# Kernel tuning notes

Measured on AMD Instinct MI355X. Metric: run time of the kernel, lower is better.

Reference implementation:

```python
import jax, jax.numpy as jnp
import numpy as np

N_NODES = 100000
N_EDGES = 1600000
IN_DIM, HID_DIM, OUT_DIM = 128, 64, 64
NEG_SLOPE = 0.2


def _gat_layer(h_in, src, dst, W, a_src, a_dst, b, n_nodes):
    # h: [N, F_out]
    h = h_in @ W.T
    alpha_src = h @ a_src  # [N]
    alpha_dst = h @ a_dst  # [N]
    # per-edge raw attention logits (edge j->i: src=j, dst=i)
    e = jax.nn.leaky_relu(alpha_src[src] + alpha_dst[dst], NEG_SLOPE)  # [E]
    # segment softmax over incoming edges of each dst node
    m = jax.ops.segment_max(e, dst, num_segments=n_nodes)
    ex = jnp.exp(e - m[dst])
    denom = jax.ops.segment_sum(ex, dst, num_segments=n_nodes)
    alpha = ex / denom[dst]  # [E], denom > 0 thanks to self-loops
    out = jax.ops.segment_sum(h[src] * alpha[:, None], dst, num_segments=n_nodes)
    return out + b


def setup_inputs() -> dict:
    key = jax.random.key(0)
    ks = jax.random.split(key, 12)
    x = jax.random.normal(ks[0], (N_NODES, IN_DIM), dtype=jnp.float32)
    edge_index = jax.random.randint(ks[1], (2, N_EDGES), 0, N_NODES)
    edge_attr = jax.random.normal(ks[2], (N_EDGES, 1), dtype=jnp.float32)
    s1 = 1.0 / np.sqrt(IN_DIM)
    s2 = 1.0 / np.sqrt(HID_DIM)
    W1 = jax.random.normal(ks[3], (HID_DIM, IN_DIM), dtype=jnp.float32) * s1
    att_src1 = jax.random.normal(ks[4], (HID_DIM,), dtype=jnp.float32) * s2
    att_dst1 = jax.random.normal(ks[5], (HID_DIM,), dtype=jnp.float32) * s2
    b1 = jnp.zeros((HID_DIM,), dtype=jnp.float32)
    W2 = jax.random.normal(ks[6], (OUT_DIM, HID_DIM), dtype=jnp.float32) * s2
    att_src2 = jax.random.normal(ks[7], (OUT_DIM,), dtype=jnp.float32) * s2
    att_dst2 = jax.random.normal(ks[8], (OUT_DIM,), dtype=jnp.float32) * s2
    b2 = jnp.zeros((OUT_DIM,), dtype=jnp.float32)
    return {"x": x, "edge_index": edge_index, "edge_attr": edge_attr,
            "W1": W1, "att_src1": att_src1, "att_dst1": att_dst1, "b1": b1,
            "W2": W2, "att_src2": att_src2, "att_dst2": att_dst2, "b2": b2}


def reference(x, edge_index, edge_attr, W1, att_src1, att_dst1, b1,
              W2, att_src2, att_dst2, b2):
    n = x.shape[0]
    # add self-loops (PyG GATConv default); edge_attr unused (edge_dim=None)
    loop = jnp.arange(n, dtype=edge_index.dtype)
    src = jnp.concatenate([edge_index[0], loop])
    dst = jnp.concatenate([edge_index[1], loop])
    h = _gat_layer(x, src, dst, W1, att_src1, att_dst1, b1, n)
    h = jax.nn.relu(h)
    h = _gat_layer(h, src, dst, W2, att_src2, att_dst2, b2, n)
    # global_mean_pool with batch=None -> mean over all nodes, shape [1, F]
    return jnp.mean(h, axis=0, keepdims=True)
```

## Files before the change

kernel.cpp:

```cpp
#include <hip/hip_runtime.h>

#define NEG_SLOPE 0.2f
#define BSHIFT 6
#define NBMAX 2048
#define BCAP 1408
#define CHUNK 8192

__device__ __forceinline__ unsigned short f2b(float x) {
    unsigned u = __float_as_uint(x);
    u += 0x7fff + ((u >> 16) & 1);
    return (unsigned short)(u >> 16);
}
__device__ __forceinline__ float b2f(unsigned short u) {
    return __uint_as_float((unsigned)u << 16);
}

__global__ __launch_bounds__(256) void bin_fixed_kernel(
    const int* __restrict__ ei, int* __restrict__ bcnt,
    int* __restrict__ binned, int E, int NB)
{
    __shared__ int cnt1[NBMAX], rsv[NBMAX], cnt2[NBMAX];
    const int tid = threadIdx.x;
    for (int i = tid; i < NB; i += 256) { cnt1[i] = 0; cnt2[i] = 0; }
    __syncthreads();
    const int start = blockIdx.x * CHUNK;
    const int end = min(start + CHUNK, E);
    for (int i = start + tid; i < end; i += 256)
        atomicAdd(&cnt1[ei[E + i] >> BSHIFT], 1);
    __syncthreads();
    for (int i = tid; i < NB; i += 256)
        rsv[i] = cnt1[i] ? atomicAdd(&bcnt[i], cnt1[i]) : 0;
    __syncthreads();
    for (int i = start + tid; i < end; i += 256) {
        int s = ei[i], d = ei[E + i];
        int b = d >> BSHIFT;
        int r = rsv[b] + atomicAdd(&cnt2[b], 1);
        if (r < BCAP) binned[(size_t)b * BCAP + r] = (s << BSHIFT) | (d & 63);
    }
}

__global__ __launch_bounds__(256) void bscan_kernel(
    const int* __restrict__ bcnt, int* __restrict__ bbase, int NB)
{
    __shared__ int lds[256];
    const int t = threadIdx.x;
    int v[8]; int s = 0;
    #pragma unroll
    for (int j = 0; j < 8; ++j) {
        int i = t * 8 + j;
        v[j] = (i < NB) ? bcnt[i] : 0;
        s += v[j];
    }
    lds[t] = s;
    __syncthreads();
    #pragma unroll
    for (int off = 1; off < 256; off <<= 1) {
        int x = (t >= off) ? lds[t - off] : 0;
        __syncthreads();
        lds[t] += x;
        __syncthreads();
    }
    int excl = (t > 0) ? lds[t - 1] : 0;
    #pragma unroll
    for (int j = 0; j < 8; ++j) {
        int i = t * 8 + j;
        if (i < NB) { bbase[i] = excl + 64 * i; excl += v[j]; }
    }
}

__global__ __launch_bounds__(256) void bucket_csr_kernel(
    const int* __restrict__ binned, const int* __restrict__ bcnt,
    const int* __restrict__ bbase, int* __restrict__ row_ptr,
    int* __restrict__ esrc, int N)
{
    __shared__ int ldeg[64];
    __shared__ int lcur[64];
    const int b = blockIdx.x;
    const int tid = threadIdx.x;
    const int node0 = b << BSHIFT;
    const int cnt = min(bcnt[b], BCAP);
    const int base_e = bbase[b];
    const int* bp = binned + (size_t)b * BCAP;

    if (tid < 64) ldeg[tid] = (node0 + tid < N) ? 1 : 0;
    __syncthreads();
    for (int i = tid; i < cnt; i += 256)
        atomicAdd(&ldeg[bp[i] & 63], 1);
    __syncthreads();
    if (tid < 64) {
        int v = ldeg[tid];
        int inc = v;
        #pragma unroll
        for (int off = 1; off < 64; off <<= 1) {
            int t2 = __shfl_up(inc, off, 64);
            if (tid >= off) inc += t2;
        }
        int excl = inc - v;
        int node = node0 + tid;
        if (node <= N) row_ptr[node] = base_e + excl;
        if (node < N) {
            esrc[base_e + excl] = node;
            lcur[tid] = base_e + excl + 1;
        }
    }
    __syncthreads();
    for (int i = tid; i < cnt; i += 256) {
        int v = bp[i];
        int pos = atomicAdd(&lcur[v & 63], 1);
        esrc[pos] = v >> BSHIFT;
    }
}

template<int K>
__global__ __launch_bounds__(256) void gemm_attn_kernel(
    const float* __restrict__ in, const float* __restrict__ W,
    const float* __restrict__ a_src, const float* __restrict__ a_dst,
    unsigned short* __restrict__ hb, float* __restrict__ asrc,
    float* __restrict__ adst, int N)
{
    constexpr int KB = 64;
    constexpr int NKC = KB / 4;
    constexpr int LDN = 65;
    __shared__ float4 xs4[NKC * LDN];
    __shared__ float4 ws4[NKC * LDN];
    __shared__ float avs[64], avd[64];

    const int tid = threadIdx.x;
    const int node0 = blockIdx.x * 64;
    const int tf = tid & 15;
    const int tn = tid >> 4;

    if (tid < 64) { avs[tid] = a_src[tid]; avd[tid] = a_dst[tid]; }

    float acc[4][4] = {};

    for (int k0 = 0; k0 < K; k0 += KB) {
        if (k0) __syncthreads();
        for (int i = tid; i < 64 * NKC; i += 256) {
            int r = i >> 4, kc = i & 15;
            int node = node0 + r;
            float4 xv = (node < N)
                ? *(const float4*)&in[(size_t)node * K + k0 + 4 * kc]
                : make_float4(0.f, 0.f, 0.f, 0.f);
            xs4[kc * LDN + r] = xv;
            ws4[kc * LDN + r] = *(const float4*)&W[(size_t)r * K + k0 + 4 * kc];
        }
        __syncthreads();

        #pragma unroll 4
        for (int kc = 0; kc < NKC; ++kc) {
            float4 xv[4], wv[4];
            #pragma unroll
            for (int i = 0; i < 4; ++i) xv[i] = xs4[kc * LDN + 4 * tn + i];
            #pragma unroll
            for (int j = 0; j < 4; ++j) wv[j] = ws4[kc * LDN + tf + 16 * j];
            #pragma unroll
            for (int i = 0; i < 4; ++i)
                #pragma unroll
                for (int j = 0; j < 4; ++j) {
                    acc[i][j] = fmaf(xv[i].x, wv[j].x, acc[i][j]);
                    acc[i][j] = fmaf(xv[i].y, wv[j].y, acc[i][j]);
                    acc[i][j] = fmaf(xv[i].z, wv[j].z, acc[i][j]);
                    acc[i][j] = fmaf(xv[i].w, wv[j].w, acc[i][j]);
                }
        }
    }

    #pragma unroll
    for (int i = 0; i < 4; ++i) {
        const int node = node0 + 4 * tn + i;
        const bool valid = node < N;
        float vs = 0.f, vd = 0.f;
        #pragma unroll
        for (int j = 0; j < 4; ++j) {
            int f = tf + 16 * j;
            if (valid) hb[(size_t)node * 64 + f] = f2b(acc[i][j]);
            vs = fmaf(acc[i][j], avs[f], vs);
            vd = fmaf(acc[i][j], avd[f], vd);
        }
        #pragma unroll
        for (int off = 8; off >= 1; off >>= 1) {
            vs += __shfl_down(vs, off, 16);
            vd += __shfl_down(vd, off, 16);
        }
        if (tf == 0 && valid) { asrc[node] = vs; adst[node] = vd; }
    }
}

__global__ __launch_bounds__(256) void aggregate_csr_kernel(
    const int* __restrict__ row_ptr, const int* __restrict__ esrc,
    const float* __restrict__ asrc, const float* __restrict__ adst,
    const unsigned short* __restrict__ hb, const float* __restrict__ bias,
    float* __restrict__ g, int N, int do_relu)
{
    const int node = (int)((blockIdx.x * 256 + threadIdx.x) >> 4);
    const int lane = threadIdx.x & 15;
    if (node >= N) return;
    const int beg = row_ptr[node];
    const int end = row_ptr[node + 1];
    const float ad = adst[node];
    float a0 = 0.f, a1 = 0.f, a2 = 0.f, a3 = 0.f, wsum = 0.f;
    int p = beg;
    for (; p + 4 <= end; p += 4) {
        int s[4]; ushort4 r[4]; float l[4];
        #pragma unroll
        for (int j = 0; j < 4; ++j) s[j] = esrc[p + j];
        #pragma unroll
        for (int j = 0; j < 4; ++j)
            r[j] = *(const ushort4*)(hb + (size_t)s[j] * 64 + lane * 4);
        #pragma unroll
        for (int j = 0; j < 4; ++j) l[j] = asrc[s[j]] + ad;
        #pragma unroll
        for (int j = 0; j < 4; ++j) {
            float ll = (l[j] > 0.f) ? l[j] : NEG_SLOPE * l[j];
            float w = __expf(ll);
            wsum += w;
            a0 = fmaf(w, b2f(r[j].x), a0);
            a1 = fmaf(w, b2f(r[j].y), a1);
            a2 = fmaf(w, b2f(r[j].z), a2);
            a3 = fmaf(w, b2f(r[j].w), a3);
        }
    }
    for (; p < end; ++p) {
        int s = esrc[p];
        ushort4 r = *(const ushort4*)(hb + (size_t)s * 64 + lane * 4);
        float l = asrc[s] + ad;
        l = (l > 0.f) ? l : NEG_SLOPE * l;
        float w = __expf(l);
        wsum += w;
        a0 = fmaf(w, b2f(r.x), a0);
        a1 = fmaf(w, b2f(r.y), a1);
        a2 = fmaf(w, b2f(r.z), a2);
        a3 = fmaf(w, b2f(r.w), a3);
    }
    const float inv = 1.0f / wsum;
    float4 v = make_float4(a0 * inv, a1 * inv, a2 * inv, a3 * inv);
    if (bias) {
        v.x += bias[lane * 4 + 0]; v.y += bias[lane * 4 + 1];
        v.z += bias[lane * 4 + 2]; v.w += bias[lane * 4 + 3];
    }
    if (do_relu) {
        v.x = fmaxf(v.x, 0.f); v.y = fmaxf(v.y, 0.f);
        v.z = fmaxf(v.z, 0.f); v.w = fmaxf(v.w, 0.f);
    }
    *(float4*)&g[(size_t)node * 64 + lane * 4] = v;
}

__global__ __launch_bounds__(256) void pool_kernel(
    const float* __restrict__ g, const float* __restrict__ b2,
    float* __restrict__ out, int N)
{
    __shared__ float red[256];
    const int f = threadIdx.x & 63;
    const int sub = threadIdx.x >> 6;
    float acc = 0.f;
    for (int n = blockIdx.x * 4 + sub; n < N; n += gridDim.x * 4)
        acc += g[(size_t)n * 64 + f];
    red[threadIdx.x] = acc;
    __syncthreads();
    if (threadIdx.x < 64) {
        float s = red[f] + red[64 + f] + red[128 + f] + red[192 + f];
        atomicAdd(out + f, s * (1.0f / (float)N));
        if (blockIdx.x == 0) atomicAdd(out + f, b2[f]);
    }
}

extern "C" void kernel_launch(void* const* d_in, const int* in_sizes, int n_in,
                              void* d_out, int out_size, void* d_ws, size_t ws_size,
                              hipStream_t stream) {
    const float* x   = (const float*)d_in[0];
    const int*   ei  = (const int*)d_in[1];
    const float* W1  = (const float*)d_in[3];
    const float* as1 = (const float*)d_in[4];
    const float* ad1 = (const float*)d_in[5];
    const float* b1  = (const float*)d_in[6];
    const float* W2  = (const float*)d_in[7];
    const float* as2 = (const float*)d_in[8];
    const float* ad2 = (const float*)d_in[9];
    const float* b2  = (const float*)d_in[10];
    float* out = (float*)d_out;

    const int N = in_sizes[0] / 128;
    const int E = in_sizes[1] / 2;
    const int Etot = E + N;
    const int NB = (N + 63) >> BSHIFT;

    auto align4 = [](size_t v) { return (v + 3) & ~(size_t)3; };
    float* ws    = (float*)d_ws;
    size_t off = 0;
    unsigned short* hb = (unsigned short*)(ws + off); off += align4((size_t)N * 32);
    float* g     = ws + off; off += align4((size_t)N * 64);
    float* asrc  = ws + off; off += align4(N);
    float* adst  = ws + off; off += align4(N);
    int* row_ptr = (int*)(ws + off); off += align4(N + 1);
    int* bcnt    = (int*)(ws + off); off += NBMAX;
    int* bbase   = (int*)(ws + off); off += NBMAX;
    int* esrc    = (int*)(ws + off); off += align4(Etot);
    int* binned  = (int*)g;

    const int gemm_blocks  = (N + 63) / 64;
    const int chunk_blocks = (E + CHUNK - 1) / CHUNK;
    const int agg_blocks   = (int)(((size_t)N * 16 + 255) / 256);

    hipMemsetAsync(out, 0, 64 * sizeof(float), stream);
    hipMemsetAsync(bcnt, 0, NB * sizeof(int), stream);

    bin_fixed_kernel<<<chunk_blocks, 256, 0, stream>>>(ei, bcnt, binned, E, NB);
    bscan_kernel<<<1, 256, 0, stream>>>(bcnt, bbase, NB);
    bucket_csr_kernel<<<NB, 256, 0, stream>>>(binned, bcnt, bbase, row_ptr, esrc, N);

    gemm_attn_kernel<128><<<gemm_blocks, 256, 0, stream>>>(x, W1, as1, ad1, hb, asrc, adst, N);
    aggregate_csr_kernel<<<agg_blocks, 256, 0, stream>>>(row_ptr, esrc, asrc, adst, hb, b1, g, N, 1);

    gemm_attn_kernel<64><<<gemm_blocks, 256, 0, stream>>>(g, W2, as2, ad2, hb, asrc, adst, N);
    aggregate_csr_kernel<<<agg_blocks, 256, 0, stream>>>(row_ptr, esrc, asrc, adst, hb, nullptr, g, N, 0);

    pool_kernel<<<512, 256, 0, stream>>>(g, b2, out, N);
}
```

Baseline: 311.9 us.

## Bin edges with global atomics and register-prefetch next GEMM K-chunk

The LDS-histogram chunked binning kernel becomes a one-thread-per-edge kernel that takes bucket slots directly from global atomics, and the bucket scan now clamps each count to the bucket capacity. Separately, the GEMM kernel loads the next K-chunk of inputs and weights into registers while it computes the current chunk, so global-load latency overlaps with the FMAs. The binning change trades per-block LDS reservation for heavy global atomic contention on about 1563 bucket counters, and edge order inside a bucket becomes nondeterministic. The prefetch raises register use, which may lower occupancy.

```diff
diff --git a/kernel.cpp b/kernel.cpp
--- a/kernel.cpp
+++ b/kernel.cpp
@@ -4,7 +4,6 @@
 #define BSHIFT 6
 #define NBMAX 2048
 #define BCAP 1408
-#define CHUNK 8192
 
 __device__ __forceinline__ unsigned short f2b(float x) {
     unsigned u = __float_as_uint(x);
@@ -15,28 +14,16 @@
     return __uint_as_float((unsigned)u << 16);
 }
 
-__global__ __launch_bounds__(256) void bin_fixed_kernel(
+__global__ __launch_bounds__(256) void bin_global_kernel(
     const int* __restrict__ ei, int* __restrict__ bcnt,
-    int* __restrict__ binned, int E, int NB)
-{
-    __shared__ int cnt1[NBMAX], rsv[NBMAX], cnt2[NBMAX];
-    const int tid = threadIdx.x;
-    for (int i = tid; i < NB; i += 256) { cnt1[i] = 0; cnt2[i] = 0; }
-    __syncthreads();
-    const int start = blockIdx.x * CHUNK;
-    const int end = min(start + CHUNK, E);
-    for (int i = start + tid; i < end; i += 256)
-        atomicAdd(&cnt1[ei[E + i] >> BSHIFT], 1);
-    __syncthreads();
-    for (int i = tid; i < NB; i += 256)
-        rsv[i] = cnt1[i] ? atomicAdd(&bcnt[i], cnt1[i]) : 0;
-    __syncthreads();
-    for (int i = start + tid; i < end; i += 256) {
-        int s = ei[i], d = ei[E + i];
-        int b = d >> BSHIFT;
-        int r = rsv[b] + atomicAdd(&cnt2[b], 1);
-        if (r < BCAP) binned[(size_t)b * BCAP + r] = (s << BSHIFT) | (d & 63);
-    }
+    int* __restrict__ binned, int E)
+{
+    int i = blockIdx.x * 256 + threadIdx.x;
+    if (i >= E) return;
+    int s = ei[i], d = ei[E + i];
+    int b = d >> BSHIFT;
+    int r = atomicAdd(&bcnt[b], 1);
+    if (r < BCAP) binned[(size_t)b * BCAP + r] = (s << BSHIFT) | (d & 63);
 }
 
 __global__ __launch_bounds__(256) void bscan_kernel(
@@ -48,7 +35,7 @@
     #pragma unroll
     for (int j = 0; j < 8; ++j) {
         int i = t * 8 + j;
-        v[j] = (i < NB) ? bcnt[i] : 0;
+        v[j] = (i < NB) ? min(bcnt[i], BCAP) : 0;
         s += v[j];
     }
     lds[t] = s;
@@ -120,7 +107,9 @@
 {
     constexpr int KB = 64;
     constexpr int NKC = KB / 4;
+    constexpr int NC = K / KB;
     constexpr int LDN = 65;
+    constexpr int SIT = 64 * NKC / 256;
     __shared__ float4 xs4[NKC * LDN];
     __shared__ float4 ws4[NKC * LDN];
     __shared__ float avs[64], avd[64];
@@ -133,19 +122,41 @@
     if (tid < 64) { avs[tid] = a_src[tid]; avd[tid] = a_dst[tid]; }
 
     float acc[4][4] = {};
-
-    for (int k0 = 0; k0 < K; k0 += KB) {
-        if (k0) __syncthreads();
-        for (int i = tid; i < 64 * NKC; i += 256) {
-            int r = i >> 4, kc = i & 15;
-            int node = node0 + r;
-            float4 xv = (node < N)
-                ? *(const float4*)&in[(size_t)node * K + k0 + 4 * kc]
-                : make_float4(0.f, 0.f, 0.f, 0.f);
-            xs4[kc * LDN + r] = xv;
-            ws4[kc * LDN + r] = *(const float4*)&W[(size_t)r * K + k0 + 4 * kc];
-        }
-        __syncthreads();
+    float4 px[SIT], pw[SIT];
+
+    #pragma unroll
+    for (int it = 0; it < SIT; ++it) {
+        int i = tid + 256 * it;
+        int r = i >> 4, kc = i & 15;
+        int node = node0 + r;
+        px[it] = (node < N) ? *(const float4*)&in[(size_t)node * K + 4 * kc]
+                            : make_float4(0.f, 0.f, 0.f, 0.f);
+        pw[it] = *(const float4*)&W[(size_t)r * K + 4 * kc];
+    }
+    #pragma unroll
+    for (int it = 0; it < SIT; ++it) {
+        int i = tid + 256 * it;
+        int r = i >> 4, kc = i & 15;
+        xs4[kc * LDN + r] = px[it];
+        ws4[kc * LDN + r] = pw[it];
+    }
+    __syncthreads();
+
+    #pragma unroll
+    for (int c = 0; c < NC; ++c) {
+        if (c + 1 < NC) {
+            const int k0 = (c + 1) * KB;
+            #pragma unroll
+            for (int it = 0; it < SIT; ++it) {
+                int i = tid + 256 * it;
+                int r = i >> 4, kc = i & 15;
+                int node = node0 + r;
+                px[it] = (node < N)
+                    ? *(const float4*)&in[(size_t)node * K + k0 + 4 * kc]
+                    : make_float4(0.f, 0.f, 0.f, 0.f);
+                pw[it] = *(const float4*)&W[(size_t)r * K + k0 + 4 * kc];
+            }
+        }
 
         #pragma unroll 4
         for (int kc = 0; kc < NKC; ++kc) {
@@ -163,6 +174,18 @@
                     acc[i][j] = fmaf(xv[i].z, wv[j].z, acc[i][j]);
                     acc[i][j] = fmaf(xv[i].w, wv[j].w, acc[i][j]);
                 }
+        }
+
+        if (c + 1 < NC) {
+            __syncthreads();
+            #pragma unroll
+            for (int it = 0; it < SIT; ++it) {
+                int i = tid + 256 * it;
+                int r = i >> 4, kc = i & 15;
+                xs4[kc * LDN + r] = px[it];
+                ws4[kc * LDN + r] = pw[it];
+            }
+            __syncthreads();
         }
     }
 
@@ -298,14 +321,14 @@
     int* esrc    = (int*)(ws + off); off += align4(Etot);
     int* binned  = (int*)g;
 
-    const int gemm_blocks  = (N + 63) / 64;
-    const int chunk_blocks = (E + CHUNK - 1) / CHUNK;
-    const int agg_blocks   = (int)(((size_t)N * 16 + 255) / 256);
+    const int gemm_blocks = (N + 63) / 64;
+    const int edge_blocks = (E + 255) / 256;
+    const int agg_blocks  = (int)(((size_t)N * 16 + 255) / 256);
 
     hipMemsetAsync(out, 0, 64 * sizeof(float), stream);
     hipMemsetAsync(bcnt, 0, NB * sizeof(int), stream);
 
-    bin_fixed_kernel<<<chunk_blocks, 256, 0, stream>>>(ei, bcnt, binned, E, NB);
+    bin_global_kernel<<<edge_blocks, 256, 0, stream>>>(ei, bcnt, binned, E);
     bscan_kernel<<<1, 256, 0, stream>>>(bcnt, bbase, NB);
     bucket_csr_kernel<<<NB, 256, 0, stream>>>(binned, bcnt, bbase, row_ptr, esrc, N);
 
```

New measurement: 522.7 us. 67.6% more time.
